# Optimization experiments

Measured on AMD Instinct MI355X. Metric: run time of the kernel, lower is better.

## Reference

```python
import jax, jax.numpy as jnp
import numpy as np

N, D, H = 100000, 128, 8
C = D // H
E = 800000
NEG_SLOPE = 0.2


def setup_inputs() -> dict:
    key = jax.random.key(0)
    k1, k2, k3, k4, k5, k6 = jax.random.split(key, 6)
    x = jax.random.normal(k1, (N, D), dtype=jnp.float32)
    edge_index = jax.random.randint(k2, (2, E), 0, N, dtype=jnp.int64)
    # GATConv params: shared linear (single node-feature input), per-head attention vectors, bias
    W = jax.random.normal(k3, (D, H * C), dtype=jnp.float32) * (1.0 / np.sqrt(D))
    att_src = jax.random.normal(k4, (H, C), dtype=jnp.float32) * 0.1
    att_dst = jax.random.normal(k5, (H, C), dtype=jnp.float32) * 0.1
    bias = jnp.zeros((H * C,), dtype=jnp.float32)
    return {"x": x, "edge_index": edge_index, "W": W, "att_src": att_src, "att_dst": att_dst, "bias": bias}


def reference(x, edge_index, W, att_src, att_dst, bias):
    # PyG GATConv default: add self-loops
    loops = jnp.tile(jnp.arange(N, dtype=edge_index.dtype), (2, 1))  # [2, N]
    ei = jnp.concatenate([edge_index, loops], axis=1)                # [2, E+N]
    src, dst = ei[0], ei[1]

    h = (x @ W).reshape(N, H, C)                    # [N, H, C]
    a_src = jnp.einsum('nhc,hc->nh', h, att_src)    # [N, H]
    a_dst = jnp.einsum('nhc,hc->nh', h, att_dst)    # [N, H]

    logits = jax.nn.leaky_relu(a_src[src] + a_dst[dst], negative_slope=NEG_SLOPE)  # [Etot, H]

    # segment softmax grouped by destination node (every node has a self-loop -> non-empty)
    mx = jax.ops.segment_max(logits, dst, num_segments=N)   # [N, H]
    ex = jnp.exp(logits - mx[dst])                           # [Etot, H]
    denom = jax.ops.segment_sum(ex, dst, num_segments=N)    # [N, H]
    alpha = ex / (denom[dst] + 1e-16)                        # [Etot, H]

    msg = h[src] * alpha[:, :, None]                         # [Etot, H, C]
    out = jax.ops.segment_sum(msg, dst, num_segments=N)      # [N, H, C]
    out = out.reshape(N, H * C) + bias                       # concat heads
    return out, ei, alpha
```

## Files before the change

kernel.cpp:

```cpp
#include <hip/hip_runtime.h>
#include <hip/hip_bf16.h>
#include <cstdint>

#define N_NODES 100000
#define DIM 128
#define HEADS 8
#define CH 16
#define NEDGE 800000
#define ETOT (NEDGE + N_NODES)
#define NEG_SLOPE 0.2f
#define CAP 64

typedef __attribute__((ext_vector_type(8))) short bf16x8;
typedef __attribute__((ext_vector_type(4))) float f32x4;

__device__ __forceinline__ float leaky(float v) {
    return v >= 0.f ? v : NEG_SLOPE * v;
}

__device__ __forceinline__ void split2(float w, ushort& hi, ushort& lo) {
    __hip_bfloat16 bh = __float2bfloat16(w);
    float r = w - __bfloat162float(bh);
    __hip_bfloat16 bl = __float2bfloat16(r);
    hi = *(ushort*)&bh;
    lo = *(ushort*)&bl;
}

#define NCOLS 144
#define LDK   136
#define MT    128

__global__ __launch_bounds__(512, 4) void gemm_kernel(
    const float* __restrict__ x, const float* __restrict__ W,
    const float* __restrict__ att_src, const float* __restrict__ att_dst,
    __hip_bfloat16* __restrict__ h, float* __restrict__ a_src,
    float* __restrict__ a_dst)
{
    __shared__ ushort Whi[NCOLS * LDK];
    __shared__ ushort Wlo[NCOLS * LDK];
    const int tid = threadIdx.x;

    {
        const int n  = tid >> 2;
        const int kq = (tid & 3) * 32;
        #pragma unroll
        for (int j = 0; j < 32; j += 2) {
            const int k = kq + j;
            float w0 = W[(size_t)k * DIM + n];
            float w1 = W[(size_t)(k + 1) * DIM + n];
            ushort h0, l0, h1, l1;
            split2(w0, h0, l0);
            split2(w1, h1, l1);
            *(uint*)&Whi[n * LDK + k] = (uint)h0 | ((uint)h1 << 16);
            *(uint*)&Wlo[n * LDK + k] = (uint)l0 | ((uint)l1 << 16);
        }
    }
    if (tid < 64) {
        const int t  = tid >> 2;
        const int kq = (tid & 3) * 32;
        const int hd = t & 7;
        const float* av = ((t < 8) ? att_src : att_dst) + hd * CH;
        float avr[CH];
        #pragma unroll
        for (int c = 0; c < CH; ++c) avr[c] = av[c];
        const int nrow = 128 + t;
        for (int j = 0; j < 32; j += 2) {
            const int k = kq + j;
            const float* wp0 = &W[(size_t)k * DIM + hd * CH];
            const float* wp1 = wp0 + DIM;
            float s0 = 0.f, s1 = 0.f;
            #pragma unroll
            for (int c = 0; c < CH; ++c) { s0 += wp0[c] * avr[c]; s1 += wp1[c] * avr[c]; }
            ushort h0, l0, h1, l1;
            split2(s0, h0, l0);
            split2(s1, h1, l1);
            *(uint*)&Whi[nrow * LDK + k] = (uint)h0 | ((uint)h1 << 16);
            *(uint*)&Wlo[nrow * LDK + k] = (uint)l0 | ((uint)l1 << 16);
        }
    }
    __syncthreads();

    const int w    = tid >> 6;
    const int lane = tid & 63;
    const int r    = lane & 15;
    const int g    = lane >> 4;
    const long arow = (long)blockIdx.x * MT + w * 16 + r;
    const bool avalid = arow < N_NODES;

    f32x4 acc[9] = {};
    #pragma unroll
    for (int ks = 0; ks < 4; ++ks) {
        const int k0 = ks * 32 + g * 8;
        float xv[8];
        if (avalid) {
            *(float4*)&xv[0] = *(const float4*)&x[arow * DIM + k0];
            *(float4*)&xv[4] = *(const float4*)&x[arow * DIM + k0 + 4];
        } else {
            #pragma unroll
            for (int j = 0; j < 8; ++j) xv[j] = 0.f;
        }
        bf16x8 ahi, alo;
        #pragma unroll
        for (int j = 0; j < 8; ++j) {
            ushort hb, lb;
            split2(xv[j], hb, lb);
            ahi[j] = (short)hb;
            alo[j] = (short)lb;
        }
        #pragma unroll
        for (int nt = 0; nt < 9; ++nt) {
            const int nr = nt * 16 + r;
            bf16x8 bhi = *(const bf16x8*)&Whi[nr * LDK + k0];
            bf16x8 blo = *(const bf16x8*)&Wlo[nr * LDK + k0];
            acc[nt] = __builtin_amdgcn_mfma_f32_16x16x32_bf16(ahi, bhi, acc[nt], 0, 0, 0);
            acc[nt] = __builtin_amdgcn_mfma_f32_16x16x32_bf16(alo, bhi, acc[nt], 0, 0, 0);
            acc[nt] = __builtin_amdgcn_mfma_f32_16x16x32_bf16(ahi, blo, acc[nt], 0, 0, 0);
        }
    }

    const long orow0 = (long)blockIdx.x * MT + w * 16 + g * 4;
    #pragma unroll
    for (int q = 0; q < 4; ++q) {
        const long orow = orow0 + q;
        if (orow < N_NODES) {
            #pragma unroll
            for (int nt = 0; nt < 8; ++nt)
                h[orow * DIM + nt * 16 + r] = __float2bfloat16(acc[nt][q]);
            const float av = acc[8][q];
            if (r < 8) a_src[orow * HEADS + r]       = av;
            else       a_dst[orow * HEADS + (r - 8)] = av;
        }
    }
}

__global__ __launch_bounds__(256) void edge_kernel(const int* __restrict__ edge_index,
                                                   float* __restrict__ ei_out,
                                                   int* __restrict__ fill,
                                                   int* __restrict__ ebuf) {
    int e = blockIdx.x * 256 + threadIdx.x;
    if (e >= ETOT) return;
    int s, d;
    if (e < NEDGE) { s = edge_index[e]; d = edge_index[NEDGE + e]; }
    else           { s = d = e - NEDGE; }
    ei_out[e]        = (float)s;
    ei_out[ETOT + e] = (float)d;
    int pos = atomicAdd(&fill[d], 1);
    if (pos < CAP) ebuf[d * CAP + pos] = e;
}

__global__ __launch_bounds__(256) void gather_kernel(const int* __restrict__ edge_index,
                                                     const int* __restrict__ fill,
                                                     const int* __restrict__ ebuf,
                                                     const __hip_bfloat16* __restrict__ h,
                                                     const float* __restrict__ a_src,
                                                     const float* __restrict__ a_dst,
                                                     const float* __restrict__ bias,
                                                     float* __restrict__ alpha_out,
                                                     float* __restrict__ out) {
    __shared__ int   s_s[4][CAP];
    __shared__ int   s_e[4][CAP];
    __shared__ float s_al[4][CAP][9];
    const int tid  = threadIdx.x;
    const int w    = tid >> 6;
    const int lane = tid & 63;
    const int n    = blockIdx.x * 4 + w;
    const int head = lane >> 3, c = lane & 7;
    const int chb  = head * CH + c * 2;
    const int dn   = min(fill[n], CAP);
    const float ad = a_dst[n * HEADS + head];

    if (lane < dn) {
        int e = ebuf[n * CAP + lane];
        s_e[w][lane] = e;
        s_s[w][lane] = (e < NEDGE) ? edge_index[e] : e - NEDGE;
    }
    __syncthreads();

    float m = -1e30f, dsum = 0.f;
    for (int i = c; i < dn; i += 8) {
        float lg = leaky(a_src[s_s[w][i] * HEADS + head] + ad);
        s_al[w][i][head] = lg;
        float mn = fmaxf(m, lg);
        dsum = dsum * __expf(m - mn) + __expf(lg - mn);
        m = mn;
    }
    #pragma unroll
    for (int off = 1; off < 8; off <<= 1) {
        float mo = __shfl_xor(m, off);
        float so = __shfl_xor(dsum, off);
        float mn = fmaxf(m, mo);
        dsum = dsum * __expf(m - mn) + so * __expf(mo - mn);
        m = mn;
    }
    const float rdinv = 1.f / (dsum + 1e-16f);
    for (int i = c; i < dn; i += 8) {
        float al = __expf(s_al[w][i][head] - m) * rdinv;
        s_al[w][i][head] = al;
        alpha_out[(size_t)s_e[w][i] * HEADS + head] = al;
    }
    __syncthreads();

    float ax = 0.f, ay = 0.f;
    int i = 0;
    for (; i + 8 <= dn; i += 8) {
        unsigned hv[8]; float av[8];
        #pragma unroll
        for (int q = 0; q < 8; ++q) {
            int s = s_s[w][i + q];
            hv[q] = *(const unsigned*)(h + (size_t)s * DIM + chb);
            av[q] = s_al[w][i + q][head];
        }
        #pragma unroll
        for (int q = 0; q < 8; ++q) {
            ax += __uint_as_float(hv[q] << 16) * av[q];
            ay += __uint_as_float(hv[q] & 0xffff0000u) * av[q];
        }
    }
    for (; i < dn; ++i) {
        unsigned hv = *(const unsigned*)(h + (size_t)s_s[w][i] * DIM + chb);
        float al = s_al[w][i][head];
        ax += __uint_as_float(hv << 16) * al;
        ay += __uint_as_float(hv & 0xffff0000u) * al;
    }
    float2 b = *(const float2*)&bias[chb];
    float2 r; r.x = ax + b.x; r.y = ay + b.y;
    *(float2*)&out[(size_t)n * DIM + chb] = r;
}

extern "C" void kernel_launch(void* const* d_in, const int* in_sizes, int n_in,
                              void* d_out, int out_size, void* d_ws, size_t ws_size,
                              hipStream_t stream) {
    const float* x          = (const float*)d_in[0];
    const int*   edge_index = (const int*)d_in[1];
    const float* W          = (const float*)d_in[2];
    const float* att_src    = (const float*)d_in[3];
    const float* att_dst    = (const float*)d_in[4];
    const float* bias       = (const float*)d_in[5];

    float* out       = (float*)d_out;
    float* ei_out    = out + (size_t)N_NODES * DIM;
    float* alpha_out = ei_out + 2 * (size_t)ETOT;

    __hip_bfloat16* h = (__hip_bfloat16*)d_ws;
    float* a_src = (float*)(h + (size_t)N_NODES * DIM);
    float* a_dst = a_src + (size_t)N_NODES * HEADS;
    int*   fill  = (int*)(a_dst + (size_t)N_NODES * HEADS);
    int*   ebuf  = fill + N_NODES;

    hipMemsetAsync(fill, 0, (size_t)N_NODES * sizeof(int), stream);

    edge_kernel<<<(ETOT + 255) / 256, 256, 0, stream>>>(edge_index, ei_out, fill, ebuf);
    gemm_kernel<<<(N_NODES + MT - 1) / MT, 512, 0, stream>>>(x, W, att_src, att_dst,
                                                             h, a_src, a_dst);
    gather_kernel<<<N_NODES / 4, 256, 0, stream>>>(edge_index, fill, ebuf, h,
                                                   a_src, a_dst, bias, alpha_out, out);
}
```

Before: 314.9 us.

## Prefetch neighbor features early and restructure per-node softmax in aggregation kernel

The aggregation kernel now issues gathers of the first 16 neighbor feature rows right after loading edge indices, so their latency overlaps the softmax computation. Block-wide __syncthreads are replaced by wave-local LDS waitcnt fences, since each wave owns its node. The online max/sum softmax becomes a two-pass max-then-exp, with normalization deferred to the output and alpha writes moved to the end. 32-bit unsigned byte-offset addressing replaces 64-bit index math. The prefetch array adds register pressure, and the wave-local fences depend on each wave only touching its own LDS slots.

Result: faster. 299.0 us (-5.1%).

```diff
diff --git a/kernel.cpp b/kernel.cpp
--- a/kernel.cpp
+++ b/kernel.cpp
@@ -10,12 +10,18 @@
 #define ETOT (NEDGE + N_NODES)
 #define NEG_SLOPE 0.2f
 #define CAP 64
+#define PRE 16
 
 typedef __attribute__((ext_vector_type(8))) short bf16x8;
 typedef __attribute__((ext_vector_type(4))) float f32x4;
 
 __device__ __forceinline__ float leaky(float v) {
     return v >= 0.f ? v : NEG_SLOPE * v;
+}
+
+__device__ __forceinline__ void wave_lds_fence() {
+    asm volatile("s_waitcnt lgkmcnt(0)" ::: "memory");
+    __builtin_amdgcn_sched_barrier(0);
 }
 
 __device__ __forceinline__ void split2(float w, ushort& hi, ushort& lo) {
@@ -167,64 +173,72 @@
     const int head = lane >> 3, c = lane & 7;
     const int chb  = head * CH + c * 2;
     const int dn   = min(fill[n], CAP);
-    const float ad = a_dst[n * HEADS + head];
+    const float ad = a_dst[(uint)n * HEADS + head];
 
     if (lane < dn) {
-        int e = ebuf[n * CAP + lane];
+        int e = ebuf[(uint)n * CAP + lane];
         s_e[w][lane] = e;
         s_s[w][lane] = (e < NEDGE) ? edge_index[e] : e - NEDGE;
     }
-    __syncthreads();
-
-    float m = -1e30f, dsum = 0.f;
+    wave_lds_fence();
+
+    const char* hb  = (const char*)h;
+    const uint  cho = (uint)chb * 2u;
+    const int npre = min(dn, PRE);
+    unsigned hv[PRE];
+    #pragma unroll
+    for (int q = 0; q < PRE; ++q) {
+        if (q < npre)
+            hv[q] = *(const unsigned*)(hb + ((uint)s_s[w][q] * 256u + cho));
+    }
+
+    const char* asb = (const char*)a_src;
+    const uint  hdo = (uint)(head << 2);
+    float m = -1e30f;
     for (int i = c; i < dn; i += 8) {
-        float lg = leaky(a_src[s_s[w][i] * HEADS + head] + ad);
+        float as = *(const float*)(asb + ((uint)s_s[w][i] * 32u + hdo));
+        float lg = leaky(as + ad);
         s_al[w][i][head] = lg;
-        float mn = fmaxf(m, lg);
-        dsum = dsum * __expf(m - mn) + __expf(lg - mn);
-        m = mn;
-    }
-    #pragma unroll
-    for (int off = 1; off < 8; off <<= 1) {
-        float mo = __shfl_xor(m, off);
-        float so = __shfl_xor(dsum, off);
-        float mn = fmaxf(m, mo);
-        dsum = dsum * __expf(m - mn) + so * __expf(mo - mn);
-        m = mn;
-    }
+        m = fmaxf(m, lg);
+    }
+    #pragma unroll
+    for (int off = 1; off < 8; off <<= 1)
+        m = fmaxf(m, __shfl_xor(m, off));
+
+    float dsum = 0.f;
+    for (int i = c; i < dn; i += 8) {
+        float ex = __expf(s_al[w][i][head] - m);
+        s_al[w][i][head] = ex;
+        dsum += ex;
+    }
+    #pragma unroll
+    for (int off = 1; off < 8; off <<= 1)
+        dsum += __shfl_xor(dsum, off);
     const float rdinv = 1.f / (dsum + 1e-16f);
-    for (int i = c; i < dn; i += 8) {
-        float al = __expf(s_al[w][i][head] - m) * rdinv;
-        s_al[w][i][head] = al;
-        alpha_out[(size_t)s_e[w][i] * HEADS + head] = al;
-    }
-    __syncthreads();
+    wave_lds_fence();
 
     float ax = 0.f, ay = 0.f;
-    int i = 0;
-    for (; i + 8 <= dn; i += 8) {
-        unsigned hv[8]; float av[8];
-        #pragma unroll
-        for (int q = 0; q < 8; ++q) {
-            int s = s_s[w][i + q];
-            hv[q] = *(const unsigned*)(h + (size_t)s * DIM + chb);
-            av[q] = s_al[w][i + q][head];
-        }
-        #pragma unroll
-        for (int q = 0; q < 8; ++q) {
-            ax += __uint_as_float(hv[q] << 16) * av[q];
-            ay += __uint_as_float(hv[q] & 0xffff0000u) * av[q];
-        }
-    }
-    for (; i < dn; ++i) {
-        unsigned hv = *(const unsigned*)(h + (size_t)s_s[w][i] * DIM + chb);
-        float al = s_al[w][i][head];
-        ax += __uint_as_float(hv << 16) * al;
-        ay += __uint_as_float(hv & 0xffff0000u) * al;
-    }
+    #pragma unroll
+    for (int q = 0; q < PRE; ++q) {
+        if (q < npre) {
+            float ex = s_al[w][q][head];
+            ax += __uint_as_float(hv[q] << 16) * ex;
+            ay += __uint_as_float(hv[q] & 0xffff0000u) * ex;
+        }
+    }
+    for (int i = PRE; i < dn; ++i) {
+        unsigned hq = *(const unsigned*)(hb + ((uint)s_s[w][i] * 256u + cho));
+        float ex = s_al[w][i][head];
+        ax += __uint_as_float(hq << 16) * ex;
+        ay += __uint_as_float(hq & 0xffff0000u) * ex;
+    }
+    ax *= rdinv; ay *= rdinv;
     float2 b = *(const float2*)&bias[chb];
     float2 r; r.x = ax + b.x; r.y = ay + b.y;
-    *(float2*)&out[(size_t)n * DIM + chb] = r;
+    *(float2*)&out[(uint)n * DIM + chb] = r;
+
+    for (int i = c; i < dn; i += 8)
+        alpha_out[(uint)s_e[w][i] * 8u + head] = s_al[w][i][head] * rdinv;
 }
 
 extern "C" void kernel_launch(void* const* d_in, const int* in_sizes, int n_in,
```
